# Kernel tuning notes

Hardware: AMD Instinct MI355X
Metric: run time of the kernel (lower is better)

The kernel has to match this reference:

```python
import jax, jax.numpy as jnp
import numpy as np


def setup_inputs() -> dict:
    key = jax.random.key(0)
    ks = jax.random.split(key, 7)
    B, Nc, Nt = 4, 2048, 2048
    D = 512          # key_size == representation_size
    H, E = 8, 64     # num_heads, head_dim = D // H
    return {
        "keys": jax.random.normal(ks[0], (B, Nc, D), dtype=jnp.float32),
        "values": jax.random.normal(ks[1], (B, Nc, D), dtype=jnp.float32),
        "query": jax.random.normal(ks[2], (B, Nt, D), dtype=jnp.float32),
        "Wk": jax.random.normal(ks[3], (H, D, E), dtype=jnp.float32) * 0.02,
        "Wv": jax.random.normal(ks[4], (H, D, E), dtype=jnp.float32) * 0.02,
        "Wq": jax.random.normal(ks[5], (H, D, E), dtype=jnp.float32) * 0.02,
        "Wout": jax.random.normal(ks[6], (D, D), dtype=jnp.float32) * 0.02,
    }


def reference(keys, values, query, Wk, Wv, Wq, Wout):
    # Batched per-head projections (replaces the per-head Python loop)
    k = jnp.einsum("bnd,hde->bhne", keys, Wk)    # [B,H,Nc,E]
    v = jnp.einsum("bnd,hde->bhne", values, Wv)  # [B,H,Nc,E]
    q = jnp.einsum("bnd,hde->bhne", query, Wq)   # [B,H,Nt,E]
    head_dim = q.shape[-1]
    # NOTE: original scales by head_dim (query.size()[2]), not sqrt(head_dim)
    scores = jnp.einsum("bhqe,bhke->bhqk", q, k) / head_dim
    attn = jax.nn.softmax(scores, axis=-1)
    out = jnp.einsum("bhqk,bhke->bhqe", attn, v)  # [B,H,Nt,E]
    # concat over heads (head-major feature order, matches torch.cat(dim=-1))
    B, H, Nt, E = out.shape
    out = jnp.transpose(out, (0, 2, 1, 3)).reshape(B, Nt, H * E)
    # final Linear (no bias): x @ Wout^T
    return out @ Wout.T
```

## Files before the change

kernel.cpp:

```cpp
#include <hip/hip_runtime.h>

#define B_   4
#define H_   8
#define NSEQ 2048
#define D_   512
#define E_   64

typedef __bf16 bf16x8 __attribute__((ext_vector_type(8)));
typedef float  f32x4  __attribute__((ext_vector_type(4)));
typedef float  f32x16 __attribute__((ext_vector_type(16)));

__device__ __forceinline__ unsigned short f2b(float f) {
    __bf16 h = (__bf16)f;
    return __builtin_bit_cast(unsigned short, h);
}
__device__ __forceinline__ unsigned pk2(float a, float b) {
    return (unsigned)f2b(a) | ((unsigned)f2b(b) << 16);
}
__device__ __forceinline__ bf16x8 ld_frag(const unsigned short* p) {
    return *reinterpret_cast<const bf16x8*>(p);
}
__device__ __forceinline__ void async_copy16(const void* g, const unsigned short* l) {
    __builtin_amdgcn_global_load_lds(
        (const __attribute__((address_space(1))) unsigned int*)g,
        (__attribute__((address_space(3))) unsigned int*)l, 16, 0, 0);
}

__device__ __forceinline__ int lds_blk(int r, int s) {
    int lr = r >> 1;
    return lr * 128 + (((((r & 1) << 3) | s) ^ (lr & 15)) << 3);
}
#define STAGE_SRC(r0, l, row, slot)                                            \
    {   int lr_ = ((r0) >> 1) + ((l) >> 4);                                    \
        int B_x = ((l) & 15) ^ (lr_ & 15);                                     \
        row = (lr_ << 1) | (B_x >> 3);  slot = B_x & 7; }

__device__ __forceinline__ int lds_blk32(int r, int s) {
    int lr = r >> 2;
    return lr * 128 + (((((r & 3) << 2) | s) ^ (lr & 15)) << 3);
}
#define STAGE_SRC32(r0, l, row, slot)                                          \
    {   int lr_ = ((r0) >> 2) + ((l) >> 4);                                    \
        int B_x = ((l) & 15) ^ (lr_ & 15);                                     \
        row = (lr_ << 2) | (B_x >> 2);  slot = B_x & 3; }

__global__ __launch_bounds__(256)
void prep_kernel(const float* __restrict__ q, const float* __restrict__ k,
                 const float* __restrict__ v,
                 const float* __restrict__ Wk, const float* __restrict__ Wv,
                 const float* __restrict__ Wq, const float* __restrict__ Wo,
                 unsigned short* __restrict__ qx, unsigned short* __restrict__ kx,
                 unsigned short* __restrict__ vx,
                 unsigned short* __restrict__ okt, unsigned short* __restrict__ ovt,
                 unsigned short* __restrict__ oqt, unsigned short* __restrict__ oo) {
    const int y = blockIdx.y;
    if (y == 3) {
        int idx = blockIdx.x * 256 + threadIdx.x;
        int hh = idx >> 15, rem = idx & 32767, d = rem >> 6, e = rem & 63;
        int t = hh * 32768 + e * 512 + d;
        okt[t] = f2b(Wk[idx]);
        ovt[t] = f2b(Wv[idx]);
        oqt[t] = f2b(Wq[idx] * 0.015625f);
        oo[idx] = f2b(Wo[idx]);
        return;
    }
    const float* src = y == 0 ? q : (y == 1 ? k : v);
    unsigned short* dst = y == 0 ? qx : (y == 1 ? kx : vx);
    #pragma unroll
    for (int i = 0; i < 4; ++i) {
        int e = blockIdx.x * 4096 + i * 1024 + threadIdx.x * 4;
        float4 f = *reinterpret_cast<const float4*>(src + e);
        *reinterpret_cast<ushort4*>(dst + e) =
            make_ushort4(f2b(f.x), f2b(f.y), f2b(f.z), f2b(f.w));
    }
}

__global__ __launch_bounds__(256, 3)
void proj_gemm(const unsigned short* __restrict__ qx,
               const unsigned short* __restrict__ kx,
               const unsigned short* __restrict__ vx,
               const unsigned short* __restrict__ wqt,
               const unsigned short* __restrict__ wkt,
               const unsigned short* __restrict__ wvt,
               unsigned short* __restrict__ qb, unsigned short* __restrict__ kb,
               unsigned short* __restrict__ vtb) {
    const int m0  = blockIdx.x * 128;
    const int no0 = blockIdx.y * 128;
    const int which = blockIdx.z;
    const int tid = threadIdx.x;
    const int wave = tid >> 6, lane = tid & 63;
    const int quad = lane >> 4, l16 = lane & 15;
    const int wr = wave >> 1, wc = wave & 1;

    const unsigned short* X = which == 0 ? qx : (which == 1 ? kx : vx);
    const unsigned short* W = which == 0 ? wqt : (which == 1 ? wkt : wvt);

    __shared__ unsigned short SM[16384];
    unsigned short* Ab = SM;
    unsigned short* Bb = SM + 8192;

    const unsigned short* Xp = X + (size_t)m0 * D_;
    const unsigned short* Wp = W + (size_t)no0 * D_;

    int rowS[2], slS[2];
    #pragma unroll
    for (int i = 0; i < 2; ++i) STAGE_SRC32(wave * 32 + i * 16, lane, rowS[i], slS[i])

    #define PROJ_STAGE(kt, buf)                                                \
        {   _Pragma("unroll")                                                  \
            for (int i = 0; i < 2; ++i)                                        \
                async_copy16(Xp + (size_t)rowS[i] * D_ + (kt) * 32 + slS[i] * 8, \
                             Ab + (buf) * 4096 + (wave * 32 + i * 16) * 32);   \
            _Pragma("unroll")                                                  \
            for (int i = 0; i < 2; ++i)                                        \
                async_copy16(Wp + (size_t)rowS[i] * D_ + (kt) * 32 + slS[i] * 8, \
                             Bb + (buf) * 4096 + (wave * 32 + i * 16) * 32);   \
        }

    PROJ_STAGE(0, 0)
    __syncthreads();

    const f32x4 z = {0.f, 0.f, 0.f, 0.f};
    f32x4 acc[4][4];
    #pragma unroll
    for (int i = 0; i < 4; ++i)
        #pragma unroll
        for (int j = 0; j < 4; ++j) acc[i][j] = z;

    for (int kt = 0; kt < 16; ++kt) {
        const int cur = kt & 1;
        if (kt + 1 < 16) PROJ_STAGE(kt + 1, 1 - cur)
        bf16x8 bfr[4];
        #pragma unroll
        for (int nt = 0; nt < 4; ++nt)
            bfr[nt] = ld_frag(&Bb[cur * 4096 +
                                  lds_blk32(wc * 64 + nt * 16 + l16, quad)]);
        #pragma unroll
        for (int mt = 0; mt < 4; ++mt) {
            bf16x8 af = ld_frag(&Ab[cur * 4096 +
                                    lds_blk32(wr * 64 + mt * 16 + l16, quad)]);
            #pragma unroll
            for (int nt = 0; nt < 4; ++nt)
                acc[mt][nt] = __builtin_amdgcn_mfma_f32_16x16x32_bf16(
                    af, bfr[nt], acc[mt][nt], 0, 0, 0);
        }
        __syncthreads();
    }

    if (which != 2) {
        unsigned short* Y = (which == 0 ? qb : kb);
        unsigned short (*Os)[136] = reinterpret_cast<unsigned short(*)[136]>(SM);
        #pragma unroll
        for (int h = 0; h < 2; ++h) {
            if (wr == h) {
                #pragma unroll
                for (int mt = 0; mt < 4; ++mt)
                    #pragma unroll
                    for (int nt = 0; nt < 4; ++nt)
                        #pragma unroll
                        for (int r = 0; r < 4; ++r)
                            Os[mt * 16 + quad * 4 + r][wc * 64 + nt * 16 + l16] =
                                f2b(acc[mt][nt][r]);
            }
            __syncthreads();
            #pragma unroll
            for (int i = 0; i < 4; ++i) {
                int idx = tid + i * 256;
                int row = idx >> 4, seg = idx & 15;
                *reinterpret_cast<uint4*>(
                    Y + (size_t)(m0 + h * 64 + row) * D_ + no0 + seg * 8) =
                    *reinterpret_cast<const uint4*>(&Os[row][seg * 8]);
            }
            if (h == 0) __syncthreads();
        }
    } else {
        unsigned short (*Ot)[144] = reinterpret_cast<unsigned short(*)[144]>(SM);
        const int b = m0 >> 11, nloc = m0 & 2047;
        #pragma unroll
        for (int h = 0; h < 2; ++h) {
            if (wc == h) {
                #pragma unroll
                for (int mt = 0; mt < 4; ++mt)
                    #pragma unroll
                    for (int nt = 0; nt < 4; ++nt) {
                        ushort4 o = make_ushort4(
                            f2b(acc[mt][nt][0]), f2b(acc[mt][nt][1]),
                            f2b(acc[mt][nt][2]), f2b(acc[mt][nt][3]));
                        *reinterpret_cast<ushort4*>(
                            &Ot[nt * 16 + l16][wr * 64 + mt * 16 + quad * 4]) = o;
                    }
            }
            __syncthreads();
            #pragma unroll
            for (int i = 0; i < 4; ++i) {
                int idx = tid + i * 256;
                int lhe = idx >> 4, seg = idx & 15;
                int ghe = no0 + h * 64 + lhe;
                *reinterpret_cast<uint4*>(
                    vtb + ((size_t)(b * H_ + (ghe >> 6)) * E_ + (ghe & 63)) * NSEQ +
                    nloc + seg * 8) =
                    *reinterpret_cast<const uint4*>(&Ot[lhe][seg * 8]);
            }
            if (h == 0) __syncthreads();
        }
    }
    #undef PROJ_STAGE
}

__global__ __launch_bounds__(256, 3)
void attn_kernel(const unsigned short* __restrict__ qbp,
                 const unsigned short* __restrict__ kbp,
                 const unsigned short* __restrict__ vtbp,
                 unsigned short* __restrict__ aob) {
    const int L = blockIdx.x;
    const int bh = L & 31, qt = L >> 5;
    const int b = bh >> 3, h = bh & 7;
    const int n0 = qt * 64;
    const int tid = threadIdx.x;
    const int wave = tid >> 6, lane = tid & 63;
    const int wk = wave >> 1, wq = wave & 1;
    const int l32 = lane & 31, hi = lane >> 5;

    __shared__ unsigned short Ks[2][4096];
    __shared__ unsigned short Vs[2][4096];

    const unsigned short* kbase = kbp + (size_t)(b * NSEQ) * D_ + h * 64;
    const unsigned short* vbase = vtbp + (size_t)(b * H_ + h) * E_ * NSEQ;

    int rowS[2], slS[2];
    #pragma unroll
    for (int i = 0; i < 2; ++i) STAGE_SRC(wave * 16 + i * 8, lane, rowS[i], slS[i])

    bf16x8 qf[4];
    #pragma unroll
    for (int ks = 0; ks < 4; ++ks)
        qf[ks] = ld_frag(qbp + (size_t)(b * NSEQ + n0 + wq * 32 + l32) * D_ +
                         h * 64 + ks * 16 + hi * 8);

    #define ATTN_STAGE(j, buf)                                                 \
        {   _Pragma("unroll")                                                  \
            for (int i = 0; i < 2; ++i) {                                      \
                async_copy16(                                                  \
                    kbase + (size_t)((j) * 64 + rowS[i]) * D_ + slS[i] * 8,    \
                    &Ks[buf][wave * 1024 + i * 512]);                          \
                async_copy16(                                                  \
                    vbase + (size_t)rowS[i] * NSEQ + (j) * 64 + slS[i] * 8,    \
                    &Vs[buf][wave * 1024 + i * 512]);                          \
            } }

    ATTN_STAGE(0, 0)
    __syncthreads();

    f32x16 oacc[2] = {};
    float lacc = 0.f;

    for (int j = 0; j < NSEQ / 64; ++j) {
        const int cur = j & 1;
        if (j + 1 < NSEQ / 64) ATTN_STAGE(j + 1, 1 - cur)

        const unsigned short* Kc = Ks[cur];
        const unsigned short* Vc = Vs[cur];

        f32x16 sacc = {};
        #pragma unroll
        for (int ks = 0; ks < 4; ++ks) {
            bf16x8 kf = ld_frag(&Kc[lds_blk(wk * 32 + l32, ks * 2 + hi)]);
            sacc = __builtin_amdgcn_mfma_f32_32x32x16_bf16(kf, qf[ks], sacc, 0, 0, 0);
        }

        float p[16];
        #pragma unroll
        for (int r = 0; r < 16; ++r) p[r] = __expf(sacc[r]);
        lacc += ((p[0] + p[1]) + (p[2] + p[3])) + ((p[4] + p[5]) + (p[6] + p[7])) +
                (((p[8] + p[9]) + (p[10] + p[11])) + ((p[12] + p[13]) + (p[14] + p[15])));

        #pragma unroll
        for (int s = 0; s < 2; ++s) {
            unsigned x0 = pk2(p[s * 8 + 0], p[s * 8 + 1]);
            unsigned x1 = pk2(p[s * 8 + 2], p[s * 8 + 3]);
            unsigned y0 = pk2(p[s * 8 + 4], p[s * 8 + 5]);
            unsigned y1 = pk2(p[s * 8 + 6], p[s * 8 + 7]);
            asm volatile("v_permlane32_swap_b32 %0, %1" : "+v"(x0), "+v"(y0));
            asm volatile("v_permlane32_swap_b32 %0, %1" : "+v"(x1), "+v"(y1));
            uint4 u = make_uint4(x0, x1, y0, y1);
            bf16x8 pb = __builtin_bit_cast(bf16x8, u);
            #pragma unroll
            for (int eb = 0; eb < 2; ++eb) {
                bf16x8 vf = ld_frag(&Vc[lds_blk(eb * 32 + l32, wk * 4 + s * 2 + hi)]);
                oacc[eb] = __builtin_amdgcn_mfma_f32_32x32x16_bf16(
                    vf, pb, oacc[eb], 0, 0, 0);
            }
        }

        __syncthreads();
    }

    lacc += __shfl_xor(lacc, 32);
    float* Of = reinterpret_cast<float*>(&Ks[0][0]);
    float* Lf = reinterpret_cast<float*>(&Vs[0][0]);
    if (wk == 0) {
        #pragma unroll
        for (int eb = 0; eb < 2; ++eb)
            #pragma unroll
            for (int rg = 0; rg < 4; ++rg) {
                f32x4 v = {oacc[eb][rg * 4 + 0], oacc[eb][rg * 4 + 1],
                           oacc[eb][rg * 4 + 2], oacc[eb][rg * 4 + 3]};
                *reinterpret_cast<f32x4*>(
                    &Of[(wq * 32 + l32) * 64 + eb * 32 + rg * 8 + hi * 4]) = v;
            }
        if (hi == 0) Lf[wq * 32 + l32] = lacc;
    }
    __syncthreads();
    if (wk == 1) {
        const float li = 1.0f / (lacc + Lf[wq * 32 + l32]);
        unsigned short* op =
            aob + (size_t)(b * NSEQ + n0 + wq * 32 + l32) * D_ + h * 64;
        #pragma unroll
        for (int eb = 0; eb < 2; ++eb)
            #pragma unroll
            for (int rg = 0; rg < 4; ++rg) {
                const f32x4 o = *reinterpret_cast<const f32x4*>(
                    &Of[(wq * 32 + l32) * 64 + eb * 32 + rg * 8 + hi * 4]);
                ushort4 st = make_ushort4(f2b((oacc[eb][rg * 4 + 0] + o.x) * li),
                                          f2b((oacc[eb][rg * 4 + 1] + o.y) * li),
                                          f2b((oacc[eb][rg * 4 + 2] + o.z) * li),
                                          f2b((oacc[eb][rg * 4 + 3] + o.w) * li));
                *reinterpret_cast<ushort4*>(op + eb * 32 + rg * 8 + hi * 4) = st;
            }
    }
    #undef ATTN_STAGE
}

__global__ __launch_bounds__(256, 3)
void out_gemm(const unsigned short* __restrict__ A,
              const unsigned short* __restrict__ Wo,
              float* __restrict__ Out) {
    const int m0  = blockIdx.x * 128;
    const int no0 = blockIdx.y * 128;
    const int tid = threadIdx.x;
    const int wave = tid >> 6, lane = tid & 63;
    const int quad = lane >> 4, l16 = lane & 15;
    const int wr = wave >> 1, wc = wave & 1;

    __shared__ unsigned short SM[16384];
    unsigned short* Ab = SM;
    unsigned short* Bb = SM + 8192;

    const unsigned short* Ap = A + (size_t)m0 * D_;
    const unsigned short* Bp = Wo + (size_t)no0 * D_;

    int rowS[2], slS[2];
    #pragma unroll
    for (int i = 0; i < 2; ++i) STAGE_SRC32(wave * 32 + i * 16, lane, rowS[i], slS[i])

    #define OUT_STAGE(kt, buf)                                                 \
        {   _Pragma("unroll")                                                  \
            for (int i = 0; i < 2; ++i)                                        \
                async_copy16(Ap + (size_t)rowS[i] * D_ + (kt) * 32 + slS[i] * 8, \
                             Ab + (buf) * 4096 + (wave * 32 + i * 16) * 32);   \
            _Pragma("unroll")                                                  \
            for (int i = 0; i < 2; ++i)                                        \
                async_copy16(Bp + (size_t)rowS[i] * D_ + (kt) * 32 + slS[i] * 8, \
                             Bb + (buf) * 4096 + (wave * 32 + i * 16) * 32);   \
        }

    OUT_STAGE(0, 0)
    __syncthreads();

    const f32x4 z = {0.f, 0.f, 0.f, 0.f};
    f32x4 acc[4][4];
    #pragma unroll
    for (int i = 0; i < 4; ++i)
        #pragma unroll
        for (int j = 0; j < 4; ++j) acc[i][j] = z;

    for (int kt = 0; kt < 16; ++kt) {
        const int cur = kt & 1;
        if (kt + 1 < 16) OUT_STAGE(kt + 1, 1 - cur)
        bf16x8 bfr[4];
        #pragma unroll
        for (int nt = 0; nt < 4; ++nt)
            bfr[nt] = ld_frag(&Bb[cur * 4096 +
                                  lds_blk32(wc * 64 + nt * 16 + l16, quad)]);
        #pragma unroll
        for (int mt = 0; mt < 4; ++mt) {
            bf16x8 af = ld_frag(&Ab[cur * 4096 +
                                    lds_blk32(wr * 64 + mt * 16 + l16, quad)]);
            #pragma unroll
            for (int nt = 0; nt < 4; ++nt)
                acc[mt][nt] = __builtin_amdgcn_mfma_f32_16x16x32_bf16(
                    af, bfr[nt], acc[mt][nt], 0, 0, 0);
        }
        __syncthreads();
    }
    #pragma unroll
    for (int mt = 0; mt < 4; ++mt)
        #pragma unroll
        for (int nt = 0; nt < 4; ++nt)
            #pragma unroll
            for (int r = 0; r < 4; ++r)
                Out[(size_t)(m0 + wr * 64 + mt * 16 + quad * 4 + r) * D_ +
                    no0 + wc * 64 + nt * 16 + l16] = acc[mt][nt][r];
    #undef OUT_STAGE
}

extern "C" void kernel_launch(void* const* d_in, const int* in_sizes, int n_in,
                              void* d_out, int out_size, void* d_ws, size_t ws_size,
                              hipStream_t stream) {
    const float* keys   = (const float*)d_in[0];
    const float* values = (const float*)d_in[1];
    const float* query  = (const float*)d_in[2];
    const float* Wk     = (const float*)d_in[3];
    const float* Wv     = (const float*)d_in[4];
    const float* Wq     = (const float*)d_in[5];
    const float* Wout   = (const float*)d_in[6];
    float* out = (float*)d_out;

    unsigned short* ws16 = (unsigned short*)d_ws;
    const size_t XN = (size_t)B_ * NSEQ * D_;
    const size_t WN = (size_t)H_ * D_ * E_;
    unsigned short* wkt = ws16;
    unsigned short* wvt = wkt + WN;
    unsigned short* wqt = wvt + WN;
    unsigned short* wob = wqt + WN;
    unsigned short* qb  = wob + WN;
    unsigned short* kb  = qb + XN;
    unsigned short* vtb = kb + XN;
    unsigned short* aob = vtb + XN;
    unsigned short* qx  = aob + XN;
    unsigned short* kx  = qx + XN;
    unsigned short* vx  = aob;

    prep_kernel<<<dim3(1024, 4), 256, 0, stream>>>(
        query, keys, values, Wk, Wv, Wq, Wout,
        qx, kx, vx, wkt, wvt, wqt, wob);

    proj_gemm<<<dim3(64, 4, 3), 256, 0, stream>>>(
        qx, kx, vx, wqt, wkt, wvt, qb, kb, vtb);

    attn_kernel<<<dim3(1024), 256, 0, stream>>>(qb, kb, vtb, aob);

    out_gemm<<<dim3(64, 4), 256, 0, stream>>>(aob, wob, out);
}
```

Baseline: 187.4 us.

## Triple-buffer projection and output GEMM loads with explicit vmcnt waits

Changes the projection GEMM and output GEMM from double to triple buffering in LDS, prefetching two k-tiles ahead. The full __syncthreads is replaced with explicit s_waitcnt on vmcnt/lgkmcnt, raw barriers and scheduling fences. The main loop is also fully unrolled. This is meant to hide global-to-LDS load latency behind MFMA work, at the cost of 50% more LDS per block (possibly lower occupancy) and more reliance on hand-managed wait counts being correct.

```diff
diff --git a/kernel.cpp b/kernel.cpp
--- a/kernel.cpp
+++ b/kernel.cpp
@@ -43,6 +43,11 @@
     {   int lr_ = ((r0) >> 2) + ((l) >> 4);                                    \
         int B_x = ((l) & 15) ^ (lr_ & 15);                                     \
         row = (lr_ << 2) | (B_x >> 2);  slot = B_x & 3; }
+
+#define WAIT_LGKM0  asm volatile("s_waitcnt lgkmcnt(0)" ::: "memory")
+#define WAIT_VM(N)  asm volatile("s_waitcnt vmcnt(" #N ")" ::: "memory")
+#define SCHED_FENCE __builtin_amdgcn_sched_barrier(0)
+#define RAW_BARRIER __builtin_amdgcn_s_barrier()
 
 __global__ __launch_bounds__(256)
 void prep_kernel(const float* __restrict__ q, const float* __restrict__ k,
@@ -95,9 +100,9 @@
     const unsigned short* X = which == 0 ? qx : (which == 1 ? kx : vx);
     const unsigned short* W = which == 0 ? wqt : (which == 1 ? wkt : wvt);
 
-    __shared__ unsigned short SM[16384];
+    __shared__ unsigned short SM[24576];
     unsigned short* Ab = SM;
-    unsigned short* Bb = SM + 8192;
+    unsigned short* Bb = SM + 12288;
 
     const unsigned short* Xp = X + (size_t)m0 * D_;
     const unsigned short* Wp = W + (size_t)no0 * D_;
@@ -118,7 +123,11 @@
         }
 
     PROJ_STAGE(0, 0)
-    __syncthreads();
+    PROJ_STAGE(1, 1)
+    WAIT_VM(4);
+    SCHED_FENCE;
+    RAW_BARRIER;
+    SCHED_FENCE;
 
     const f32x4 z = {0.f, 0.f, 0.f, 0.f};
     f32x4 acc[4][4];
@@ -127,9 +136,10 @@
         #pragma unroll
         for (int j = 0; j < 4; ++j) acc[i][j] = z;
 
+    #pragma unroll
     for (int kt = 0; kt < 16; ++kt) {
-        const int cur = kt & 1;
-        if (kt + 1 < 16) PROJ_STAGE(kt + 1, 1 - cur)
+        const int cur = kt % 3;
+        if (kt + 2 < 16) PROJ_STAGE(kt + 2, (kt + 2) % 3)
         bf16x8 bfr[4];
         #pragma unroll
         for (int nt = 0; nt < 4; ++nt)
@@ -144,7 +154,12 @@
                 acc[mt][nt] = __builtin_amdgcn_mfma_f32_16x16x32_bf16(
                     af, bfr[nt], acc[mt][nt], 0, 0, 0);
         }
-        __syncthreads();
+        WAIT_LGKM0;
+        if (kt + 2 < 16)      { WAIT_VM(4); }
+        else if (kt + 1 < 16) { WAIT_VM(0); }
+        SCHED_FENCE;
+        RAW_BARRIER;
+        SCHED_FENCE;
     }
 
     if (which != 2) {
@@ -342,9 +357,9 @@
     const int quad = lane >> 4, l16 = lane & 15;
     const int wr = wave >> 1, wc = wave & 1;
 
-    __shared__ unsigned short SM[16384];
+    __shared__ unsigned short SM[24576];
     unsigned short* Ab = SM;
-    unsigned short* Bb = SM + 8192;
+    unsigned short* Bb = SM + 12288;
 
     const unsigned short* Ap = A + (size_t)m0 * D_;
     const unsigned short* Bp = Wo + (size_t)no0 * D_;
@@ -365,7 +380,11 @@
         }
 
     OUT_STAGE(0, 0)
-    __syncthreads();
+    OUT_STAGE(1, 1)
+    WAIT_VM(4);
+    SCHED_FENCE;
+    RAW_BARRIER;
+    SCHED_FENCE;
 
     const f32x4 z = {0.f, 0.f, 0.f, 0.f};
     f32x4 acc[4][4];
@@ -374,9 +393,10 @@
         #pragma unroll
         for (int j = 0; j < 4; ++j) acc[i][j] = z;
 
+    #pragma unroll
     for (int kt = 0; kt < 16; ++kt) {
-        const int cur = kt & 1;
-        if (kt + 1 < 16) OUT_STAGE(kt + 1, 1 - cur)
+        const int cur = kt % 3;
+        if (kt + 2 < 16) OUT_STAGE(kt + 2, (kt + 2) % 3)
         bf16x8 bfr[4];
         #pragma unroll
         for (int nt = 0; nt < 4; ++nt)
@@ -391,7 +411,12 @@
                 acc[mt][nt] = __builtin_amdgcn_mfma_f32_16x16x32_bf16(
                     af, bfr[nt], acc[mt][nt], 0, 0, 0);
         }
-        __syncthreads();
+        WAIT_LGKM0;
+        if (kt + 2 < 16)      { WAIT_VM(4); }
+        else if (kt + 1 < 16) { WAIT_VM(0); }
+        SCHED_FENCE;
+        RAW_BARRIER;
+        SCHED_FENCE;
     }
     #pragma unroll
     for (int mt = 0; mt < 4; ++mt)
```

Measured after the change: 185.5 us. Within noise of the previous version (-1.0%).
